# Optimization experiments

Measured on AMD Instinct MI355X. Metric: run time of the kernel, lower is better.

The kernel has to match this reference:

```python
import jax, jax.numpy as jnp
import numpy as np

N_HEAD = 16
D_HEAD = 64
HIDDEN = 1024
T = 2048
B = 4


def setup_inputs() -> dict:
    key = jax.random.key(0)
    k1, k2, k3, k4, k5 = jax.random.split(key, 5)
    qkv_out = (2 * N_HEAD + 1) * D_HEAD  # 2112
    return {
        "x": jax.random.normal(k1, (B, T, HIDDEN), dtype=jnp.float32),
        "w_qkv": jax.random.normal(k2, (qkv_out, HIDDEN), dtype=jnp.float32) * (HIDDEN ** -0.5),
        "b_qkv": jax.random.normal(k3, (qkv_out,), dtype=jnp.float32) * 0.02,
        "w_out": jax.random.normal(k4, (HIDDEN, D_HEAD), dtype=jnp.float32) * (D_HEAD ** -0.5),
        "b_out": jax.random.normal(k5, (HIDDEN,), dtype=jnp.float32) * 0.02,
    }


def reference(x, w_qkv, b_qkv, w_out, b_out):
    bs, t, h = x.shape
    scale = D_HEAD ** -0.5
    qkv = x @ w_qkv.T + b_qkv  # [b, t, (2H+1)*dh]
    q, k, v = jnp.split(qkv, [N_HEAD * D_HEAD, 2 * N_HEAD * D_HEAD], axis=-1)
    q = q.reshape(bs, t, N_HEAD, D_HEAD)
    k = k.reshape(bs, t, N_HEAD, D_HEAD)
    v = v.reshape(bs, t, D_HEAD)  # single V head shared across all heads
    # attn_score: [b, h, i, j]
    attn_score = jnp.einsum("bihd,bjhd->bhij", q, k) * scale
    # causal mask: -inf above diagonal
    causal = jnp.triu(jnp.full((t, t), -jnp.inf, dtype=attn_score.dtype), 1)
    attn_score = attn_score + causal
    attn_prob = jax.nn.softmax(attn_score, axis=-1)  # dropout is identity in eval
    # shared V across heads: [b,h,i,j] x [b,j,d] -> [b,h,i,d]
    attn_vec = jnp.einsum("bhij,bjd->bhid", attn_prob, v)
    m_attn_vec = jnp.mean(attn_vec, axis=1)  # mean over heads -> [b, t, d_head]
    out = m_attn_vec @ w_out.T + b_out  # [b, t, hidden]
    return out, attn_vec
```

## Files before the change

kernel.cpp:

```cpp
#include <hip/hip_runtime.h>
#include <hip/hip_bf16.h>
#include <math.h>

#define NHEAD 16
#define DHEAD 64
#define HIDDEN 1024
#define TSEQ 2048
#define BATCH 4
#define QKV_OUT 2112
#define BT (BATCH * TSEQ)

typedef __attribute__((ext_vector_type(8))) short bf16x8;
typedef __attribute__((ext_vector_type(4))) float floatx4;

static __device__ __forceinline__ short f2bf(float x) {
  __hip_bfloat16 h = __float2bfloat16(x);
  return *reinterpret_cast<short*>(&h);
}

#define MFMA16(a, b, c) __builtin_amdgcn_mfma_f32_16x16x32_bf16(a, b, c, 0, 0, 0)

__global__ __launch_bounds__(256) void f32_to_bf16(
    const float* __restrict__ src, short* __restrict__ dst, int n) {
  const int i = (blockIdx.x * 256 + threadIdx.x) * 8;
  if (i >= n) return;
  float4 a = *(const float4*)&src[i];
  float4 b = *(const float4*)&src[i + 4];
  short o[8];
  o[0] = f2bf(a.x); o[1] = f2bf(a.y); o[2] = f2bf(a.z); o[3] = f2bf(a.w);
  o[4] = f2bf(b.x); o[5] = f2bf(b.y); o[6] = f2bf(b.z); o[7] = f2bf(b.w);
  *(uint4*)&dst[i] = *(uint4*)o;
}

#define QK_BM 128
#define QK_BN 64
#define QK_BK 64

template <typename OUT_T>
__global__ __launch_bounds__(256) void gemm_mfma_bf16(
    const short* __restrict__ A, const short* __restrict__ B,
    const float* __restrict__ bias, OUT_T* __restrict__ C,
    int M, int N, int K) {
  __shared__ short As[QK_BM][72];
  __shared__ short Bs[QK_BN][72];

  const int nbx = N / QK_BN;
  const int nwg = nbx * (M / QK_BM);
  const int cpx = nwg >> 3;
  const int bid = (int)blockIdx.x;
  const int lid = (bid & 7) * cpx + (bid >> 3);
  const int bx = lid % nbx;
  const int by = lid / nbx;

  const int tid = threadIdx.x;
  const int lane = tid & 63;
  const int wv = tid >> 6;
  const int ln = lane & 15;
  const int grp = lane >> 4;
  const int wm = wv >> 1;
  const int wn = wv & 1;
  const int rowbase = by * QK_BM;
  const int colbase = bx * QK_BN;

  const int ar = tid >> 1, ac = (tid & 1) * 32;
  const int br = tid >> 2, bc = (tid & 3) * 16;

  floatx4 acc[4][2];
#pragma unroll
  for (int m = 0; m < 4; ++m)
#pragma unroll
    for (int n = 0; n < 2; ++n) acc[m][n] = (floatx4){0.f, 0.f, 0.f, 0.f};

  const short* ap = A + (size_t)(rowbase + ar) * K + ac;
  const short* bp = B + (size_t)(colbase + br) * K + bc;

  uint4 a0 = *(const uint4*)(ap + 0);
  uint4 a1 = *(const uint4*)(ap + 8);
  uint4 a2 = *(const uint4*)(ap + 16);
  uint4 a3 = *(const uint4*)(ap + 24);
  uint4 b0 = *(const uint4*)(bp + 0);
  uint4 b1 = *(const uint4*)(bp + 8);

  for (int k0 = 0; k0 < K; k0 += QK_BK) {
    __syncthreads();
    *(uint4*)&As[ar][ac + 0] = a0;
    *(uint4*)&As[ar][ac + 8] = a1;
    *(uint4*)&As[ar][ac + 16] = a2;
    *(uint4*)&As[ar][ac + 24] = a3;
    *(uint4*)&Bs[br][bc + 0] = b0;
    *(uint4*)&Bs[br][bc + 8] = b1;
    __syncthreads();

    if (k0 + QK_BK < K) {
      ap += QK_BK;
      bp += QK_BK;
      a0 = *(const uint4*)(ap + 0);
      a1 = *(const uint4*)(ap + 8);
      a2 = *(const uint4*)(ap + 16);
      a3 = *(const uint4*)(ap + 24);
      b0 = *(const uint4*)(bp + 0);
      b1 = *(const uint4*)(bp + 8);
    }

#pragma unroll
    for (int ks = 0; ks < 2; ++ks) {
      bf16x8 bfrag[2];
#pragma unroll
      for (int n = 0; n < 2; ++n)
        bfrag[n] = *(const bf16x8*)&Bs[wn * 32 + n * 16 + ln][ks * 32 + grp * 8];
#pragma unroll
      for (int m = 0; m < 4; ++m) {
        bf16x8 af = *(const bf16x8*)&As[wm * 64 + m * 16 + ln][ks * 32 + grp * 8];
#pragma unroll
        for (int n = 0; n < 2; ++n)
          acc[m][n] = MFMA16(af, bfrag[n], acc[m][n]);
      }
    }
  }

#pragma unroll
  for (int n = 0; n < 2; ++n) {
    const int col = colbase + wn * 32 + n * 16 + ln;
    const float bv = bias[col];
#pragma unroll
    for (int m = 0; m < 4; ++m) {
#pragma unroll
      for (int r = 0; r < 4; ++r) {
        const int row = rowbase + wm * 64 + m * 16 + grp * 4 + r;
        const float v = acc[m][n][r] + bv;
        if constexpr (sizeof(OUT_T) == 2)
          C[(size_t)row * N + col] = f2bf(v);
        else
          C[(size_t)row * N + col] = v;
      }
    }
  }
}

__global__ __launch_bounds__(256) void transpose_v(
    const short* __restrict__ qkv, short* __restrict__ vt) {
  __shared__ short tile[64][72];
  const int tt = blockIdx.x;
  const int b = blockIdx.y;
  const int tid = threadIdx.x;
  const int li = tid >> 2;
  const int lc = (tid & 3) * 16;

  const short* src = qkv + (size_t)(b * TSEQ + tt * 64 + li) * QKV_OUT + 2048 + lc;
  *(uint4*)&tile[li][lc] = *(const uint4*)src;
  *(uint4*)&tile[li][lc + 8] = *(const uint4*)(src + 8);
  __syncthreads();
  short tmp[16];
#pragma unroll
  for (int u = 0; u < 16; ++u) tmp[u] = tile[lc + u][li];
  short* dst = vt + (size_t)(b * 64 + li) * TSEQ + tt * 64 + lc;
  *(uint4*)dst = *(uint4*)&tmp[0];
  *(uint4*)(dst + 8) = *(uint4*)&tmp[8];
}

#define QB 128

__global__ __launch_bounds__(512) void attn_partial(
    const short* __restrict__ qkv, const short* __restrict__ vt,
    float* __restrict__ attn_vec, float* __restrict__ pO,
    float* __restrict__ pL) {
  __shared__ short Ks[64][72];
  __shared__ short Vt[64][72];
  __shared__ short Ps[128][72];

  const int x = (int)gridDim.x - 1 - (int)blockIdx.x;
  int it, jc;
  if (x < 8) {
    it = x; jc = 0;
  } else {
    it = 8 + ((x - 8) >> 1); jc = (x - 8) & 1;
  }
  const int jstart = jc * 16;
  const int jend = min(jstart + 16, 2 * it + 2);

  const int tid = threadIdx.x;
  const int h = blockIdx.y;
  const int b = blockIdx.z;
  const int lane = tid & 63;
  const int wv = tid >> 6;
  const int ln = lane & 15;
  const int grp = lane >> 4;
  const int qbase = wv * 16;
  const int sr = tid >> 3;
  const int sc = (tid & 7) * 8;
  const float CEXP = 0.18033688f;

  const short* qptr =
      qkv + (size_t)(b * TSEQ + it * QB + qbase + ln) * QKV_OUT + h * 64;
  const bf16x8 bq0 = *(const bf16x8*)(qptr + grp * 8);
  const bf16x8 bq1 = *(const bf16x8*)(qptr + 32 + grp * 8);

  floatx4 oT[4];
#pragma unroll
  for (int m = 0; m < 4; ++m) oT[m] = (floatx4){0.f, 0.f, 0.f, 0.f};
  float lsum = 0.f;

  const short* ks0 =
      qkv + (size_t)(b * TSEQ + jstart * 64 + sr) * QKV_OUT + 1024 + h * 64 + sc;
  const short* vs0 = vt + (size_t)(b * 64 + sr) * TSEQ + jstart * 64 + sc;
  uint4 kr = *(const uint4*)ks0;
  uint4 vr = *(const uint4*)vs0;

  for (int jt = jstart; jt < jend; ++jt) {
    __syncthreads();
    *(uint4*)&Ks[sr][sc] = kr;
    *(uint4*)&Vt[sr][sc] = vr;
    __syncthreads();

    if (jt + 1 < jend) {
      const short* kn =
          qkv + (size_t)(b * TSEQ + (jt + 1) * 64 + sr) * QKV_OUT + 1024 + h * 64 + sc;
      const short* vn = vt + (size_t)(b * 64 + sr) * TSEQ + (jt + 1) * 64 + sc;
      kr = *(const uint4*)kn;
      vr = *(const uint4*)vn;
    }

    const int qg = it * QB + qbase;
    if (qg + 15 >= jt * 64) {
      floatx4 st[4];
      __builtin_amdgcn_s_setprio(1);
#pragma unroll
      for (int m = 0; m < 4; ++m) {
        bf16x8 ak0 = *(const bf16x8*)&Ks[m * 16 + ln][grp * 8];
        bf16x8 ak1 = *(const bf16x8*)&Ks[m * 16 + ln][32 + grp * 8];
        floatx4 a = (floatx4){0.f, 0.f, 0.f, 0.f};
        a = MFMA16(ak0, bq0, a);
        a = MFMA16(ak1, bq1, a);
        st[m] = a;
      }
      __builtin_amdgcn_s_setprio(0);

      const int dj = qg + ln - jt * 64;
      if (dj < 63) {
#pragma unroll
        for (int m = 0; m < 4; ++m)
#pragma unroll
          for (int r = 0; r < 4; ++r)
            if (m * 16 + grp * 4 + r > dj) st[m][r] = -INFINITY;
      }

#pragma unroll
      for (int m = 0; m < 4; ++m) {
        float p0 = exp2f(CEXP * st[m][0]);
        float p1 = exp2f(CEXP * st[m][1]);
        float p2 = exp2f(CEXP * st[m][2]);
        float p3 = exp2f(CEXP * st[m][3]);
        lsum += (p0 + p1) + (p2 + p3);
        short pk[4] = {f2bf(p0), f2bf(p1), f2bf(p2), f2bf(p3)};
        *(uint2*)&Ps[qbase + ln][m * 16 + grp * 4] = *(uint2*)pk;
      }

      bf16x8 bp0 = *(const bf16x8*)&Ps[qbase + ln][grp * 8];
      bf16x8 bp1 = *(const bf16x8*)&Ps[qbase + ln][32 + grp * 8];
      __builtin_amdgcn_s_setprio(1);
#pragma unroll
      for (int m = 0; m < 4; ++m) {
        bf16x8 av0 = *(const bf16x8*)&Vt[m * 16 + ln][grp * 8];
        bf16x8 av1 = *(const bf16x8*)&Vt[m * 16 + ln][32 + grp * 8];
        oT[m] = MFMA16(av0, bp0, oT[m]);
        oT[m] = MFMA16(av1, bp1, oT[m]);
      }
      __builtin_amdgcn_s_setprio(0);
    }
  }

  lsum += __shfl_xor(lsum, 16);
  lsum += __shfl_xor(lsum, 32);

  if (it < 8) {
    const float inv = 1.f / lsum;
    float* orow =
        attn_vec + ((size_t)(b * NHEAD + h) * TSEQ + it * QB + qbase + ln) * DHEAD;
#pragma unroll
    for (int m = 0; m < 4; ++m) {
      float4 o4;
      o4.x = oT[m][0] * inv;
      o4.y = oT[m][1] * inv;
      o4.z = oT[m][2] * inv;
      o4.w = oT[m][3] * inv;
      *(float4*)&orow[m * 16 + grp * 4] = o4;
    }
  } else {
    const int slot = (it - 8) * 2 + jc;
    const size_t sbase = (size_t)(b * NHEAD + h) * 16 + slot;
    float* prow = pO + sbase * 8192 + (size_t)(qbase + ln) * 64;
#pragma unroll
    for (int m = 0; m < 4; ++m) {
      float4 o4;
      o4.x = oT[m][0]; o4.y = oT[m][1]; o4.z = oT[m][2]; o4.w = oT[m][3];
      *(float4*)&prow[m * 16 + grp * 4] = o4;
    }
    if (grp == 0) pL[sbase * 128 + qbase + ln] = lsum;
  }
}

__global__ __launch_bounds__(256) void attn_combine(
    const float* __restrict__ pO, const float* __restrict__ pL,
    float* __restrict__ attn_vec) {
  const int it = 8 + blockIdx.x;
  const int h = blockIdx.y;
  const int b = blockIdx.z;
  const int q = threadIdx.x >> 1;
  const int dbase = (threadIdx.x & 1) * 32;
  const size_t base = (size_t)(b * NHEAD + h) * 16 + (it - 8) * 2;

  float4 acc[8];
#pragma unroll
  for (int u = 0; u < 8; ++u) acc[u] = (float4){0.f, 0.f, 0.f, 0.f};
  float l = 0.f;
#pragma unroll
  for (int c = 0; c < 2; ++c) {
    const float* pr = pO + (base + c) * 8192 + (size_t)q * 64 + dbase;
#pragma unroll
    for (int u = 0; u < 8; ++u) {
      float4 v = *(const float4*)&pr[u * 4];
      acc[u].x += v.x; acc[u].y += v.y; acc[u].z += v.z; acc[u].w += v.w;
    }
    l += pL[(base + c) * 128 + q];
  }
  const float inv = 1.f / l;
  float* orow =
      attn_vec + ((size_t)(b * NHEAD + h) * TSEQ + it * QB + q) * DHEAD + dbase;
#pragma unroll
  for (int u = 0; u < 8; ++u) {
    float4 o4;
    o4.x = acc[u].x * inv; o4.y = acc[u].y * inv;
    o4.z = acc[u].z * inv; o4.w = acc[u].w * inv;
    *(float4*)&orow[u * 4] = o4;
  }
}

__global__ __launch_bounds__(256) void mean_heads(
    const float* __restrict__ attn_vec, short* __restrict__ m) {
  const int gid = blockIdx.x * 256 + threadIdx.x;
  const int d2 = (gid & 31) * 2;
  const int t = (gid >> 5) & (TSEQ - 1);
  const int b = gid >> 16;
  float s0 = 0.f, s1 = 0.f;
#pragma unroll
  for (int h = 0; h < NHEAD; ++h) {
    const float* p = &attn_vec[(((size_t)(b * NHEAD + h) * TSEQ) + t) * DHEAD + d2];
    s0 += p[0];
    s1 += p[1];
  }
  short pk[2] = {f2bf(s0 * (1.f / 16.f)), f2bf(s1 * (1.f / 16.f))};
  *(uint*)&m[gid * 2] = *(uint*)pk;
}

extern "C" void kernel_launch(void* const* d_in, const int* in_sizes, int n_in,
                              void* d_out, int out_size, void* d_ws, size_t ws_size,
                              hipStream_t stream) {
  const float* x     = (const float*)d_in[0];
  const float* w_qkv = (const float*)d_in[1];
  const float* b_qkv = (const float*)d_in[2];
  const float* w_out = (const float*)d_in[3];
  const float* b_out = (const float*)d_in[4];

  float* out      = (float*)d_out;
  float* attn_vec = out + (size_t)BT * HIDDEN;

  short* qkv_bf  = (short*)d_ws;
  short* vt_bf   = qkv_bf + (size_t)BT * QKV_OUT;
  short* wout_bf = vt_bf + (size_t)BATCH * DHEAD * TSEQ;
  short* m_attn  = wout_bf + (size_t)HIDDEN * DHEAD;
  char*  xbase   = (char*)(m_attn + (size_t)BT * DHEAD);
  short* x_bf    = (short*)xbase;
  short* w_bf    = x_bf + (size_t)BT * HIDDEN;
  float* pO      = (float*)xbase;
  float* pL      = pO + (size_t)64 * 16 * 8192;

  f32_to_bf16<<<dim3(BT * HIDDEN / 8 / 256), 256, 0, stream>>>(
      x, x_bf, BT * HIDDEN);
  f32_to_bf16<<<dim3(QKV_OUT * HIDDEN / 8 / 256), 256, 0, stream>>>(
      w_qkv, w_bf, QKV_OUT * HIDDEN);
  f32_to_bf16<<<dim3(HIDDEN * DHEAD / 8 / 256), 256, 0, stream>>>(
      w_out, wout_bf, HIDDEN * DHEAD);

  gemm_mfma_bf16<short>
      <<<dim3((QKV_OUT / QK_BN) * (BT / QK_BM)), 256, 0, stream>>>(
          x_bf, w_bf, b_qkv, qkv_bf, BT, QKV_OUT, HIDDEN);

  transpose_v<<<dim3(TSEQ / 64, BATCH), 256, 0, stream>>>(qkv_bf, vt_bf);

  attn_partial<<<dim3(24, NHEAD, BATCH), 512, 0, stream>>>(
      qkv_bf, vt_bf, attn_vec, pO, pL);

  attn_combine<<<dim3(8, NHEAD, BATCH), 256, 0, stream>>>(pO, pL, attn_vec);

  mean_heads<<<dim3(BT * DHEAD / 2 / 256), 256, 0, stream>>>(attn_vec, m_attn);

  gemm_mfma_bf16<float>
      <<<dim3((HIDDEN / QK_BN) * (BT / QK_BM)), 256, 0, stream>>>(
          m_attn, wout_bf, b_out, out, BT, HIDDEN, DHEAD);
}
```

Baseline: 277.2 us.

## Rewrite bf16 GEMM with direct global-to-LDS loads, XOR swizzle, 128x128 tiles

Replaces the register-staged GEMM with one that uses global_load_lds to copy A and B tiles straight into shared memory. It uses an XOR-swizzled unpadded LDS layout to avoid bank conflicts and widens the tile from 128x64 to 128x128 so each wave computes 4x4 MFMA blocks. The aim is to cut global-to-LDS staging overhead and raise data reuse in both the QKV and output projections. The register prefetch that overlapped loads with compute is gone, and the ragged N=2112 edge now needs clamped loads and guarded stores.

```diff
diff --git a/kernel.cpp b/kernel.cpp
--- a/kernel.cpp
+++ b/kernel.cpp
@@ -19,6 +19,12 @@
 }
 
 #define MFMA16(a, b, c) __builtin_amdgcn_mfma_f32_16x16x32_bf16(a, b, c, 0, 0, 0)
+
+static __device__ __forceinline__ void gload_lds16(const void* g, void* l) {
+  __builtin_amdgcn_global_load_lds(
+      (const __attribute__((address_space(1))) void*)g,
+      (__attribute__((address_space(3))) void*)l, 16, 0, 0);
+}
 
 __global__ __launch_bounds__(256) void f32_to_bf16(
     const float* __restrict__ src, short* __restrict__ dst, int n) {
@@ -32,20 +38,20 @@
   *(uint4*)&dst[i] = *(uint4*)o;
 }
 
-#define QK_BM 128
-#define QK_BN 64
-#define QK_BK 64
+#define GBM 128
+#define GBN 128
+#define GBK 64
 
 template <typename OUT_T>
-__global__ __launch_bounds__(256) void gemm_mfma_bf16(
+__global__ __launch_bounds__(256) void gemm_bt_swz(
     const short* __restrict__ A, const short* __restrict__ B,
     const float* __restrict__ bias, OUT_T* __restrict__ C,
     int M, int N, int K) {
-  __shared__ short As[QK_BM][72];
-  __shared__ short Bs[QK_BN][72];
-
-  const int nbx = N / QK_BN;
-  const int nwg = nbx * (M / QK_BM);
+  __shared__ short As[GBM * GBK];
+  __shared__ short Bs[GBN * GBK];
+
+  const int nbx = (N + GBN - 1) / GBN;
+  const int nwg = nbx * (M / GBM);
   const int cpx = nwg >> 3;
   const int bid = (int)blockIdx.x;
   const int lid = (bid & 7) * cpx + (bid >> 3);
@@ -59,79 +65,69 @@
   const int grp = lane >> 4;
   const int wm = wv >> 1;
   const int wn = wv & 1;
-  const int rowbase = by * QK_BM;
-  const int colbase = bx * QK_BN;
-
-  const int ar = tid >> 1, ac = (tid & 1) * 32;
-  const int br = tid >> 2, bc = (tid & 3) * 16;
-
-  floatx4 acc[4][2];
+  const int rowbase = by * GBM;
+  const int colbase = bx * GBN;
+
+  const int crow = lane >> 3;
+  const int scol16 = (lane & 7) ^ crow;
+
+  floatx4 acc[4][4];
 #pragma unroll
   for (int m = 0; m < 4; ++m)
 #pragma unroll
-    for (int n = 0; n < 2; ++n) acc[m][n] = (floatx4){0.f, 0.f, 0.f, 0.f};
-
-  const short* ap = A + (size_t)(rowbase + ar) * K + ac;
-  const short* bp = B + (size_t)(colbase + br) * K + bc;
-
-  uint4 a0 = *(const uint4*)(ap + 0);
-  uint4 a1 = *(const uint4*)(ap + 8);
-  uint4 a2 = *(const uint4*)(ap + 16);
-  uint4 a3 = *(const uint4*)(ap + 24);
-  uint4 b0 = *(const uint4*)(bp + 0);
-  uint4 b1 = *(const uint4*)(bp + 8);
-
-  for (int k0 = 0; k0 < K; k0 += QK_BK) {
+    for (int n = 0; n < 4; ++n) acc[m][n] = (floatx4){0.f, 0.f, 0.f, 0.f};
+
+  for (int k0 = 0; k0 < K; k0 += GBK) {
     __syncthreads();
-    *(uint4*)&As[ar][ac + 0] = a0;
-    *(uint4*)&As[ar][ac + 8] = a1;
-    *(uint4*)&As[ar][ac + 16] = a2;
-    *(uint4*)&As[ar][ac + 24] = a3;
-    *(uint4*)&Bs[br][bc + 0] = b0;
-    *(uint4*)&Bs[br][bc + 8] = b1;
+#pragma unroll
+    for (int c = 0; c < 4; ++c) {
+      const int tr = (wv * 4 + c) * 8 + crow;
+      gload_lds16(A + (size_t)(rowbase + tr) * K + k0 + scol16 * 8,
+                  &As[(wv * 4 + c) * 8 * GBK]);
+      int br = colbase + tr;
+      if (br > N - 1) br = N - 1;
+      gload_lds16(B + (size_t)br * K + k0 + scol16 * 8,
+                  &Bs[(wv * 4 + c) * 8 * GBK]);
+    }
     __syncthreads();
 
-    if (k0 + QK_BK < K) {
-      ap += QK_BK;
-      bp += QK_BK;
-      a0 = *(const uint4*)(ap + 0);
-      a1 = *(const uint4*)(ap + 8);
-      a2 = *(const uint4*)(ap + 16);
-      a3 = *(const uint4*)(ap + 24);
-      b0 = *(const uint4*)(bp + 0);
-      b1 = *(const uint4*)(bp + 8);
-    }
-
 #pragma unroll
     for (int ks = 0; ks < 2; ++ks) {
-      bf16x8 bfrag[2];
-#pragma unroll
-      for (int n = 0; n < 2; ++n)
-        bfrag[n] = *(const bf16x8*)&Bs[wn * 32 + n * 16 + ln][ks * 32 + grp * 8];
-#pragma unroll
-      for (int m = 0; m < 4; ++m) {
-        bf16x8 af = *(const bf16x8*)&As[wm * 64 + m * 16 + ln][ks * 32 + grp * 8];
-#pragma unroll
-        for (int n = 0; n < 2; ++n)
+      bf16x8 bfrag[4];
+#pragma unroll
+      for (int n = 0; n < 4; ++n) {
+        const int r = wn * 64 + n * 16 + ln;
+        const int u = (ks * 4 + grp) ^ (ln & 7);
+        bfrag[n] = *(const bf16x8*)&Bs[r * GBK + u * 8];
+      }
+#pragma unroll
+      for (int m = 0; m < 4; ++m) {
+        const int r = wm * 64 + m * 16 + ln;
+        const int u = (ks * 4 + grp) ^ (ln & 7);
+        bf16x8 af = *(const bf16x8*)&As[r * GBK + u * 8];
+#pragma unroll
+        for (int n = 0; n < 4; ++n)
           acc[m][n] = MFMA16(af, bfrag[n], acc[m][n]);
       }
     }
   }
 
 #pragma unroll
-  for (int n = 0; n < 2; ++n) {
-    const int col = colbase + wn * 32 + n * 16 + ln;
-    const float bv = bias[col];
-#pragma unroll
-    for (int m = 0; m < 4; ++m) {
-#pragma unroll
-      for (int r = 0; r < 4; ++r) {
-        const int row = rowbase + wm * 64 + m * 16 + grp * 4 + r;
-        const float v = acc[m][n][r] + bv;
-        if constexpr (sizeof(OUT_T) == 2)
-          C[(size_t)row * N + col] = f2bf(v);
-        else
-          C[(size_t)row * N + col] = v;
+  for (int n = 0; n < 4; ++n) {
+    const int col = colbase + wn * 64 + n * 16 + ln;
+    if (col < N) {
+      const float bv = bias[col];
+#pragma unroll
+      for (int m = 0; m < 4; ++m) {
+#pragma unroll
+        for (int r = 0; r < 4; ++r) {
+          const int row = rowbase + wm * 64 + m * 16 + grp * 4 + r;
+          const float v = acc[m][n][r] + bv;
+          if constexpr (sizeof(OUT_T) == 2)
+            C[(size_t)row * N + col] = f2bf(v);
+          else
+            C[(size_t)row * N + col] = v;
+        }
       }
     }
   }
@@ -381,8 +377,8 @@
   f32_to_bf16<<<dim3(HIDDEN * DHEAD / 8 / 256), 256, 0, stream>>>(
       w_out, wout_bf, HIDDEN * DHEAD);
 
-  gemm_mfma_bf16<short>
-      <<<dim3((QKV_OUT / QK_BN) * (BT / QK_BM)), 256, 0, stream>>>(
+  gemm_bt_swz<short>
+      <<<dim3(((QKV_OUT + GBN - 1) / GBN) * (BT / GBM)), 256, 0, stream>>>(
           x_bf, w_bf, b_qkv, qkv_bf, BT, QKV_OUT, HIDDEN);
 
   transpose_v<<<dim3(TSEQ / 64, BATCH), 256, 0, stream>>>(qkv_bf, vt_bf);
@@ -394,7 +390,7 @@
 
   mean_heads<<<dim3(BT * DHEAD / 2 / 256), 256, 0, stream>>>(attn_vec, m_attn);
 
-  gemm_mfma_bf16<float>
-      <<<dim3((HIDDEN / QK_BN) * (BT / QK_BM)), 256, 0, stream>>>(
+  gemm_bt_swz<float>
+      <<<dim3((HIDDEN / GBN) * (BT / GBM)), 256, 0, stream>>>(
           m_attn, wout_bf, b_out, out, BT, HIDDEN, DHEAD);
 }
```

Result: slower. 284.4 us (+2.6%).
